# Kernel optimization log

Hardware: AMD Instinct MI355X
Metric: run time of the kernel (lower is better)

## Reference

```python
import jax, jax.numpy as jnp
import numpy as np

B, T, D, H, K = 8, 4096, 768, 12, 64
EPS_WKV = 1e-9
EPS_GN = 1e-5


def setup_inputs() -> dict:
    key = jax.random.key(0)
    ks = jax.random.split(key, 12)
    x = jax.random.normal(ks[0], (B, T, D), jnp.float32)
    # linear projection weights (torch nn.Linear stores [out, in]; y = x @ W.T)
    W_r = jax.random.normal(ks[1], (D, D), jnp.float32) * 0.02
    W_k = jax.random.normal(ks[2], (D, D), jnp.float32) * 0.02
    W_v = jax.random.normal(ks[3], (D, D), jnp.float32) * 0.02
    W_o = jax.random.normal(ks[4], (D, D), jnp.float32) * 0.02
    time_mix_r = jax.random.uniform(ks[5], (D,), jnp.float32)
    time_mix_k = jax.random.uniform(ks[6], (D,), jnp.float32)
    time_mix_v = jax.random.uniform(ks[7], (D,), jnp.float32)
    # around the module's init values (time_decay ~ -0.075, time_first ~ 0.15 at layer 6/12)
    time_decay = -0.075 + 0.1 * jax.random.normal(ks[8], (H, K), jnp.float32)
    time_first = 0.15 + 0.1 * jax.random.normal(ks[9], (H, K), jnp.float32)
    gn_weight = jnp.ones((D,), jnp.float32)
    gn_bias = jnp.zeros((D,), jnp.float32)
    return {
        "x": x,
        "time_mix_r": time_mix_r, "time_mix_k": time_mix_k, "time_mix_v": time_mix_v,
        "time_decay": time_decay, "time_first": time_first,
        "W_r": W_r, "W_k": W_k, "W_v": W_v, "W_o": W_o,
        "gn_weight": gn_weight, "gn_bias": gn_bias,
    }


def reference(x, time_mix_r, time_mix_k, time_mix_v, time_decay, time_first,
              W_r, W_k, W_v, W_o, gn_weight, gn_bias):
    Bx, Tx, Dx = x.shape
    Hx, Kx = time_decay.shape
    # token-shift: previous timestep (zero-initialized state)
    x_prev = jnp.concatenate([jnp.zeros_like(x[:, :1]), x[:, :-1]], axis=1)
    xr = x * time_mix_r + x_prev * (1.0 - time_mix_r)
    xk = x * time_mix_k + x_prev * (1.0 - time_mix_k)
    xv = x * time_mix_v + x_prev * (1.0 - time_mix_v)
    r = jax.nn.sigmoid(xr @ W_r.T).reshape(Bx, Tx, Hx, Kx)
    k = (xk @ W_k.T).reshape(Bx, Tx, Hx, Kx)
    v = (xv @ W_v.T).reshape(Bx, Tx, Hx, Kx)

    w = jnp.exp(-jnp.exp(time_decay))   # [H,K] decay per channel
    eu = jnp.exp(time_first)            # [H,K] bonus for current token

    def step(carry, kv_t):
        num, den = carry                # each [B,H,K]
        k_t, v_t = kv_t                 # each [B,H,K]
        ek = jnp.exp(k_t)
        wkv = (num + eu * ek * v_t) / (den + eu * ek + EPS_WKV)
        return (num * w + ek * v_t, den * w + ek), wkv

    k_tm = jnp.moveaxis(k, 1, 0)        # [T,B,H,K]
    v_tm = jnp.moveaxis(v, 1, 0)
    init = (jnp.zeros((Bx, Hx, Kx), x.dtype), jnp.zeros((Bx, Hx, Kx), x.dtype))
    _, wkv = jax.lax.scan(step, init, (k_tm, v_tm))
    out = jnp.moveaxis(wkv, 0, 1)       # [B,T,H,K]

    y = r * out                         # [B,T,H,K]
    # torch GroupNorm(H, D) on [B, D, T]: normalize each group over (K channels x T steps)
    mean = y.mean(axis=(1, 3), keepdims=True)
    var = y.var(axis=(1, 3), keepdims=True)
    y = (y - mean) * jax.lax.rsqrt(var + EPS_GN)
    y = y * gn_weight.reshape(1, 1, Hx, Kx) + gn_bias.reshape(1, 1, Hx, Kx)
    return y.reshape(Bx, Tx, Dx) @ W_o.T
```

## Files before the change

### kernel.cpp

```cpp
#include <hip/hip_runtime.h>
#include <hip/hip_bf16.h>
#include <cstdint>

#define B_ 8
#define T_ 4096
#define D_ 768
#define H_ 12
#define M_ (B_*T_)
#define CHUNKS 64
#define CLEN 64
#define WELEM (D_*D_)
#define NCH (B_*H_*64)

typedef __attribute__((ext_vector_type(8))) short bf16x8;
typedef __attribute__((ext_vector_type(4))) float f32x4;

static __device__ __forceinline__ unsigned short f2bf(float f) {
  __hip_bfloat16 h = __float2bfloat16(f);
  return __builtin_bit_cast(unsigned short, h);
}
static __device__ __forceinline__ float bf2f(unsigned short u) {
  unsigned v = ((unsigned)u) << 16;
  return __builtin_bit_cast(float, v);
}

static __device__ __forceinline__ void async16(const void* g, void* l) {
  __builtin_amdgcn_global_load_lds(
      (const __attribute__((address_space(1))) unsigned int*)g,
      (__attribute__((address_space(3))) unsigned int*)l, 16, 0, 0);
}

__global__ __launch_bounds__(256) void zero_out_kernel(float* __restrict__ out, size_t n4) {
  size_t gid = (size_t)blockIdx.x * 256 + threadIdx.x;
  if (gid < n4) *(float4*)(out + gid * 4) = make_float4(0.f, 0.f, 0.f, 0.f);
}

__global__ __launch_bounds__(256) void mix_kernel(
    const float* __restrict__ x, const float* __restrict__ tmr,
    const float* __restrict__ tmk, const float* __restrict__ tmv,
    unsigned short* __restrict__ xr, unsigned short* __restrict__ xk,
    unsigned short* __restrict__ xv) {
  size_t gid = (size_t)blockIdx.x * 256 + threadIdx.x;
  size_t idx4 = gid * 4;
  int d = (int)(idx4 % D_);
  size_t row = idx4 / D_;
  int t = (int)(row & (T_ - 1));
  float4 xc = *(const float4*)(x + idx4);
  float4 xp = make_float4(0.f, 0.f, 0.f, 0.f);
  if (t > 0) xp = *(const float4*)(x + idx4 - D_);
  float4 mr = *(const float4*)(tmr + d);
  float4 mk = *(const float4*)(tmk + d);
  float4 mv = *(const float4*)(tmv + d);
  ushort4 orr, okk, ovv;
  orr.x = f2bf(xc.x*mr.x + xp.x*(1.f-mr.x));
  orr.y = f2bf(xc.y*mr.y + xp.y*(1.f-mr.y));
  orr.z = f2bf(xc.z*mr.z + xp.z*(1.f-mr.z));
  orr.w = f2bf(xc.w*mr.w + xp.w*(1.f-mr.w));
  okk.x = f2bf(xc.x*mk.x + xp.x*(1.f-mk.x));
  okk.y = f2bf(xc.y*mk.y + xp.y*(1.f-mk.y));
  okk.z = f2bf(xc.z*mk.z + xp.z*(1.f-mk.z));
  okk.w = f2bf(xc.w*mk.w + xp.w*(1.f-mk.w));
  ovv.x = f2bf(xc.x*mv.x + xp.x*(1.f-mv.x));
  ovv.y = f2bf(xc.y*mv.y + xp.y*(1.f-mv.y));
  ovv.z = f2bf(xc.z*mv.z + xp.z*(1.f-mv.z));
  ovv.w = f2bf(xc.w*mv.w + xp.w*(1.f-mv.w));
  *(ushort4*)(xr + idx4) = orr;
  *(ushort4*)(xk + idx4) = okk;
  *(ushort4*)(xv + idx4) = ovv;
}

__global__ __launch_bounds__(256) void wconv_kernel(
    const float* __restrict__ a, const float* __restrict__ b,
    const float* __restrict__ c, const float* __restrict__ d,
    unsigned short* __restrict__ o) {
  size_t gid = (size_t)blockIdx.x * 256 + threadIdx.x;
  size_t idx4 = gid * 4;
  size_t mi = idx4 / WELEM;
  size_t off = idx4 % WELEM;
  const float* src = (mi == 0) ? a : (mi == 1) ? b : (mi == 2) ? c : d;
  float4 v = *(const float4*)(src + off);
  ushort4 u;
  u.x = f2bf(v.x); u.y = f2bf(v.y); u.z = f2bf(v.z); u.w = f2bf(v.w);
  *(ushort4*)(o + idx4) = u;
}

template<int ACT, int OBF>
__global__ __launch_bounds__(256) void gemm_nt(
    const unsigned short* __restrict__ A,
    const unsigned short* __restrict__ Bw,
    void* __restrict__ Cv, int M, int N, int Kd) {
  __shared__ __align__(16) unsigned short As[128 * 32];
  __shared__ __align__(16) unsigned short Bs[128 * 32];
  const int tid = threadIdx.x;
  const int wave = tid >> 6, lane = tid & 63;
  const int quad = lane >> 4, l16 = lane & 15;
  const int m0 = blockIdx.y * 128, n0 = blockIdx.x * 128;
  const int wm = (wave & 1) * 64, wn = (wave >> 1) * 64;

  f32x4 acc[4][4] = {};

  for (int kb = 0; kb < Kd; kb += 32) {
    __syncthreads();
#pragma unroll
    for (int j = 0; j < 2; ++j) {
      int chunk = wave * 128 + j * 64 + lane;
      int row = chunk >> 2, kc = chunk & 3;
      const unsigned short* ga = A  + ((size_t)(m0 + row) * Kd + kb + kc * 8);
      async16(ga, &As[chunk * 8]);
      const unsigned short* gb = Bw + ((size_t)(n0 + row) * Kd + kb + kc * 8);
      async16(gb, &Bs[chunk * 8]);
    }
    __syncthreads();

    bf16x8 a[4], b[4];
#pragma unroll
    for (int i = 0; i < 4; ++i)
      a[i] = *(const bf16x8*)&As[(wm + i * 16 + l16) * 32 + quad * 8];
#pragma unroll
    for (int i = 0; i < 4; ++i)
      b[i] = *(const bf16x8*)&Bs[(wn + i * 16 + l16) * 32 + quad * 8];
#pragma unroll
    for (int i = 0; i < 4; ++i)
#pragma unroll
      for (int j = 0; j < 4; ++j)
        acc[i][j] = __builtin_amdgcn_mfma_f32_16x16x32_bf16(a[i], b[j], acc[i][j], 0, 0, 0);
  }

#pragma unroll
  for (int i = 0; i < 4; ++i) {
    int rowb = m0 + wm + i * 16 + quad * 4;
#pragma unroll
    for (int j = 0; j < 4; ++j) {
      int col = n0 + wn + j * 16 + l16;
#pragma unroll
      for (int r = 0; r < 4; ++r) {
        float v = acc[i][j][r];
        if (ACT == 1) v = 1.f / (1.f + __expf(-v));
        size_t idx = (size_t)(rowb + r) * N + col;
        if (OBF) ((unsigned short*)Cv)[idx] = f2bf(v);
        else     ((float*)Cv)[idx] = v;
      }
    }
  }
}

__global__ __launch_bounds__(256) void wkv_pass1(
    const unsigned short* __restrict__ Kb, const unsigned short* __restrict__ Vb,
    const float* __restrict__ td,
    float* __restrict__ sumN, float* __restrict__ sumD) {
  int gid = blockIdx.x * 256 + threadIdx.x;
  int k = gid & 63;
  int h = (gid >> 6) % H_;
  int tmp = (gid >> 6) / H_;
  int b = tmp % B_;
  int c = tmp / B_;
  float w = __expf(-__expf(td[h * 64 + k]));
  size_t base = ((size_t)(b * T_ + c * CLEN)) * D_ + h * 64 + k;
  float num = 0.f, den = 0.f;
#pragma unroll 8
  for (int i = 0; i < CLEN; ++i) {
    float kk = bf2f(Kb[base + (size_t)i * D_]);
    float vv = bf2f(Vb[base + (size_t)i * D_]);
    float ek = __expf(kk);
    num = num * w + ek * vv;
    den = den * w + ek;
  }
  sumN[gid] = num;
  sumD[gid] = den;
}

__global__ __launch_bounds__(256) void wkv_pass2(
    const float* __restrict__ sumN, const float* __restrict__ sumD,
    const float* __restrict__ td,
    float* __restrict__ prefN, float* __restrict__ prefD,
    float* __restrict__ gstats) {
  int tid = blockIdx.x * 256 + threadIdx.x;
  if (blockIdx.x == 0 && threadIdx.x < 192) gstats[threadIdx.x] = 0.f;
  int k = tid & 63;
  int h = (tid >> 6) % H_;
  float w = __expf(-__expf(td[h * 64 + k]));
  float wL = w;
#pragma unroll
  for (int i = 0; i < 6; ++i) wL *= wL;
  float n = 0.f, d = 0.f;
  for (int c = 0; c < CHUNKS; ++c) {
    int j = c * NCH + tid;
    prefN[j] = n; prefD[j] = d;
    n = n * wL + sumN[j];
    d = d * wL + sumD[j];
  }
}

__global__ __launch_bounds__(256) void wkv_pass3(
    const unsigned short* __restrict__ Kb, const unsigned short* __restrict__ Vb,
    unsigned short* __restrict__ RY,
    const float* __restrict__ td, const float* __restrict__ tf,
    const float* __restrict__ prefN, const float* __restrict__ prefD,
    float* __restrict__ gsum, float* __restrict__ gsq) {
  int gid = blockIdx.x * 256 + threadIdx.x;
  int k = gid & 63;
  int h = (gid >> 6) % H_;
  int tmp = (gid >> 6) / H_;
  int b = tmp % B_;
  int c = tmp / B_;
  float w = __expf(-__expf(td[h * 64 + k]));
  float eu = __expf(tf[h * 64 + k]);
  float num = prefN[gid], den = prefD[gid];
  size_t base = ((size_t)(b * T_ + c * CLEN)) * D_ + h * 64 + k;
  float s1 = 0.f, s2 = 0.f;
#pragma unroll 4
  for (int i = 0; i < CLEN; ++i) {
    size_t idx = base + (size_t)i * D_;
    float kk = bf2f(Kb[idx]);
    float vv = bf2f(Vb[idx]);
    float rr = bf2f(RY[idx]);
    float ek = __expf(kk);
    float wkv = (num + eu * ek * vv) / (den + eu * ek + 1e-9f);
    unsigned short ybf = f2bf(rr * wkv);
    RY[idx] = ybf;
    float y = bf2f(ybf);
    s1 += y; s2 += y * y;
    num = num * w + ek * vv;
    den = den * w + ek;
  }
#pragma unroll
  for (int off = 32; off; off >>= 1) {
    s1 += __shfl_down(s1, off);
    s2 += __shfl_down(s2, off);
  }
  if (k == 0) {
    atomicAdd(&gsum[b * H_ + h], s1);
    atomicAdd(&gsq [b * H_ + h], s2);
  }
}

__global__ __launch_bounds__(256) void gn_kernel(
    const unsigned short* __restrict__ Y, const float* __restrict__ gsum,
    const float* __restrict__ gsq, const float* __restrict__ gw,
    const float* __restrict__ gb, unsigned short* __restrict__ Ybf) {
  size_t gid = (size_t)blockIdx.x * 256 + threadIdx.x;
  size_t idx4 = gid * 4;
  int d = (int)(idx4 % D_);
  size_t row = idx4 / D_;
  int b = (int)(row >> 12);
  int h = d >> 6;
  int g = b * H_ + h;
  const float inv = 1.f / (float)(T_ * 64);
  float mean = gsum[g] * inv;
  float var = gsq[g] * inv - mean * mean;
  float rstd = rsqrtf(var + 1e-5f);
  ushort4 yu = *(const ushort4*)(Y + idx4);
  float4 wv = *(const float4*)(gw + d);
  float4 bv = *(const float4*)(gb + d);
  ushort4 o;
  o.x = f2bf((bf2f(yu.x) - mean) * rstd * wv.x + bv.x);
  o.y = f2bf((bf2f(yu.y) - mean) * rstd * wv.y + bv.y);
  o.z = f2bf((bf2f(yu.z) - mean) * rstd * wv.z + bv.z);
  o.w = f2bf((bf2f(yu.w) - mean) * rstd * wv.w + bv.w);
  *(ushort4*)(Ybf + idx4) = o;
}

extern "C" void kernel_launch(void* const* d_in, const int* in_sizes, int n_in,
                              void* d_out, int out_size, void* d_ws, size_t ws_size,
                              hipStream_t stream) {
  (void)in_sizes; (void)n_in;
  const float* x   = (const float*)d_in[0];
  const float* tmr = (const float*)d_in[1];
  const float* tmk = (const float*)d_in[2];
  const float* tmv = (const float*)d_in[3];
  const float* td  = (const float*)d_in[4];
  const float* tf  = (const float*)d_in[5];
  const float* Wr  = (const float*)d_in[6];
  const float* Wk  = (const float*)d_in[7];
  const float* Wv  = (const float*)d_in[8];
  const float* Wo  = (const float*)d_in[9];
  const float* gw  = (const float*)d_in[10];
  const float* gb  = (const float*)d_in[11];
  float* out = (float*)d_out;

  constexpr size_t MD = (size_t)M_ * D_;
  constexpr size_t NEED = 4 * (MD * 2)
                        + (size_t)4 * WELEM * 2
                        + 4 * ((size_t)CHUNKS * NCH * 4)
                        + 1024;
  if (ws_size < NEED) {
    zero_out_kernel<<<(int)((MD / 4 + 255) / 256), 256, 0, stream>>>(out, MD / 4);
    return;
  }

  char* ws = (char*)d_ws;
  unsigned short* XR = (unsigned short*)ws; ws += MD * 2;
  unsigned short* XK = (unsigned short*)ws; ws += MD * 2;
  unsigned short* XV = (unsigned short*)ws; ws += MD * 2;
  unsigned short* Rb = (unsigned short*)ws; ws += MD * 2;
  unsigned short* Wb = (unsigned short*)ws; ws += (size_t)4 * WELEM * 2;
  float* sumN  = (float*)ws; ws += (size_t)CHUNKS * NCH * 4;
  float* sumD  = (float*)ws; ws += (size_t)CHUNKS * NCH * 4;
  float* prefN = (float*)ws; ws += (size_t)CHUNKS * NCH * 4;
  float* prefD = (float*)ws; ws += (size_t)CHUNKS * NCH * 4;
  float* gstats = (float*)ws; ws += 1024;
  unsigned short* Kb = XR;
  unsigned short* Vb = XK;
  unsigned short* Yb = XV;

  mix_kernel<<<(int)(MD / 1024), 256, 0, stream>>>(x, tmr, tmk, tmv, XR, XK, XV);
  wconv_kernel<<<(4 * WELEM / 4) / 256, 256, 0, stream>>>(Wr, Wk, Wv, Wo, Wb);

  dim3 ggrid(D_ / 128, M_ / 128);
  gemm_nt<1, 1><<<ggrid, 256, 0, stream>>>(XR, Wb,             Rb, M_, D_, D_);
  gemm_nt<0, 1><<<ggrid, 256, 0, stream>>>(XK, Wb + WELEM,     Kb, M_, D_, D_);
  gemm_nt<0, 1><<<ggrid, 256, 0, stream>>>(XV, Wb + 2 * WELEM, Vb, M_, D_, D_);

  wkv_pass1<<<(CHUNKS * NCH) / 256, 256, 0, stream>>>(Kb, Vb, td, sumN, sumD);
  wkv_pass2<<<NCH / 256, 256, 0, stream>>>(sumN, sumD, td, prefN, prefD, gstats);
  wkv_pass3<<<(CHUNKS * NCH) / 256, 256, 0, stream>>>(Kb, Vb, Rb, td, tf,
                                                      prefN, prefD, gstats, gstats + 96);
  gn_kernel<<<(int)(MD / 1024), 256, 0, stream>>>(Rb, gstats, gstats + 96, gw, gb, Yb);

  gemm_nt<0, 0><<<ggrid, 256, 0, stream>>>(Yb, Wb + 3 * WELEM, out, M_, D_, D_);
}
```

Measured before the change: 579.0 us.

## Fold token-shift mixing into concatenated weights and fuse R/K/V projections

After: 695.9 us. 20.2% more time.

```diff
diff --git a/kernel.cpp b/kernel.cpp
--- a/kernel.cpp
+++ b/kernel.cpp
@@ -9,8 +9,10 @@
 #define M_ (B_*T_)
 #define CHUNKS 64
 #define CLEN 64
-#define WELEM (D_*D_)
 #define NCH (B_*H_*64)
+#define KF 1536
+#define NF 2304
+#define TP1 (T_+1)
 
 typedef __attribute__((ext_vector_type(8))) short bf16x8;
 typedef __attribute__((ext_vector_type(4))) float f32x4;
@@ -35,118 +37,201 @@
   if (gid < n4) *(float4*)(out + gid * 4) = make_float4(0.f, 0.f, 0.f, 0.f);
 }
 
-__global__ __launch_bounds__(256) void mix_kernel(
-    const float* __restrict__ x, const float* __restrict__ tmr,
-    const float* __restrict__ tmk, const float* __restrict__ tmv,
-    unsigned short* __restrict__ xr, unsigned short* __restrict__ xk,
-    unsigned short* __restrict__ xv) {
+__global__ __launch_bounds__(256) void xpad_kernel(
+    const float* __restrict__ x, unsigned short* __restrict__ xp) {
   size_t gid = (size_t)blockIdx.x * 256 + threadIdx.x;
   size_t idx4 = gid * 4;
+  size_t row = idx4 / D_;
   int d = (int)(idx4 % D_);
-  size_t row = idx4 / D_;
-  int t = (int)(row & (T_ - 1));
-  float4 xc = *(const float4*)(x + idx4);
-  float4 xp = make_float4(0.f, 0.f, 0.f, 0.f);
-  if (t > 0) xp = *(const float4*)(x + idx4 - D_);
-  float4 mr = *(const float4*)(tmr + d);
-  float4 mk = *(const float4*)(tmk + d);
-  float4 mv = *(const float4*)(tmv + d);
-  ushort4 orr, okk, ovv;
-  orr.x = f2bf(xc.x*mr.x + xp.x*(1.f-mr.x));
-  orr.y = f2bf(xc.y*mr.y + xp.y*(1.f-mr.y));
-  orr.z = f2bf(xc.z*mr.z + xp.z*(1.f-mr.z));
-  orr.w = f2bf(xc.w*mr.w + xp.w*(1.f-mr.w));
-  okk.x = f2bf(xc.x*mk.x + xp.x*(1.f-mk.x));
-  okk.y = f2bf(xc.y*mk.y + xp.y*(1.f-mk.y));
-  okk.z = f2bf(xc.z*mk.z + xp.z*(1.f-mk.z));
-  okk.w = f2bf(xc.w*mk.w + xp.w*(1.f-mk.w));
-  ovv.x = f2bf(xc.x*mv.x + xp.x*(1.f-mv.x));
-  ovv.y = f2bf(xc.y*mv.y + xp.y*(1.f-mv.y));
-  ovv.z = f2bf(xc.z*mv.z + xp.z*(1.f-mv.z));
-  ovv.w = f2bf(xc.w*mv.w + xp.w*(1.f-mv.w));
-  *(ushort4*)(xr + idx4) = orr;
-  *(ushort4*)(xk + idx4) = okk;
-  *(ushort4*)(xv + idx4) = ovv;
-}
-
-__global__ __launch_bounds__(256) void wconv_kernel(
-    const float* __restrict__ a, const float* __restrict__ b,
-    const float* __restrict__ c, const float* __restrict__ d,
-    unsigned short* __restrict__ o) {
+  int b = (int)(row / TP1);
+  int tt = (int)(row % TP1);
+  ushort4 u = make_ushort4(0, 0, 0, 0);
+  if (tt > 0) {
+    float4 v = *(const float4*)(x + ((size_t)(b * T_ + tt - 1)) * D_ + d);
+    u.x = f2bf(v.x); u.y = f2bf(v.y); u.z = f2bf(v.z); u.w = f2bf(v.w);
+  }
+  *(ushort4*)(xp + idx4) = u;
+}
+
+__global__ __launch_bounds__(256) void wfold_kernel(
+    const float* __restrict__ Wr, const float* __restrict__ Wk,
+    const float* __restrict__ Wv,
+    const float* __restrict__ tmr, const float* __restrict__ tmk,
+    const float* __restrict__ tmv, unsigned short* __restrict__ Wcat) {
   size_t gid = (size_t)blockIdx.x * 256 + threadIdx.x;
   size_t idx4 = gid * 4;
-  size_t mi = idx4 / WELEM;
-  size_t off = idx4 % WELEM;
-  const float* src = (mi == 0) ? a : (mi == 1) ? b : (mi == 2) ? c : d;
-  float4 v = *(const float4*)(src + off);
+  int j = (int)(idx4 % KF);
+  int n = (int)(idx4 / KF);
+  int which = n / D_;
+  int nn = n % D_;
+  const float* W = (which == 0) ? Wr : (which == 1) ? Wk : Wv;
+  const float* mx = (which == 0) ? tmr : (which == 1) ? tmk : tmv;
+  int cur = (j < D_);
+  int jj = cur ? j : j - D_;
+  float4 wv = *(const float4*)(W + (size_t)nn * D_ + jj);
+  float4 mv = *(const float4*)(mx + jj);
+  float4 f;
+  f.x = cur ? mv.x : (1.f - mv.x);
+  f.y = cur ? mv.y : (1.f - mv.y);
+  f.z = cur ? mv.z : (1.f - mv.z);
+  f.w = cur ? mv.w : (1.f - mv.w);
+  ushort4 u;
+  u.x = f2bf(wv.x * f.x); u.y = f2bf(wv.y * f.y);
+  u.z = f2bf(wv.z * f.z); u.w = f2bf(wv.w * f.w);
+  *(ushort4*)(Wcat + idx4) = u;
+}
+
+__global__ __launch_bounds__(256) void woconv_kernel(
+    const float* __restrict__ w, unsigned short* __restrict__ o) {
+  size_t gid = (size_t)blockIdx.x * 256 + threadIdx.x;
+  size_t idx4 = gid * 4;
+  float4 v = *(const float4*)(w + idx4);
   ushort4 u;
   u.x = f2bf(v.x); u.y = f2bf(v.y); u.z = f2bf(v.z); u.w = f2bf(v.w);
   *(ushort4*)(o + idx4) = u;
 }
 
-template<int ACT, int OBF>
-__global__ __launch_bounds__(256) void gemm_nt(
-    const unsigned short* __restrict__ A,
-    const unsigned short* __restrict__ Bw,
-    void* __restrict__ Cv, int M, int N, int Kd) {
-  __shared__ __align__(16) unsigned short As[128 * 32];
-  __shared__ __align__(16) unsigned short Bs[128 * 32];
+__global__ __launch_bounds__(256) void gemm_fused(
+    const unsigned short* __restrict__ xpad,
+    const unsigned short* __restrict__ Wcat,
+    unsigned short* __restrict__ RKV) {
+  __shared__ __align__(16) unsigned short smem[128 * 128];
+  unsigned short* As = smem;
+  unsigned short* Bs = smem + 128 * 32;
+
+  const int flat = blockIdx.x;
+  const int xcd = flat & 7;
+  const int j8 = flat >> 3;
+  const int strip = xcd * 32 + j8 / 18;
+  const int ntile = j8 % 18;
+  const int m0 = strip * 128, n0 = ntile * 128;
+  const int b = strip >> 5;
+  const int tbase = (strip & 31) * 128;
+
   const int tid = threadIdx.x;
   const int wave = tid >> 6, lane = tid & 63;
   const int quad = lane >> 4, l16 = lane & 15;
-  const int m0 = blockIdx.y * 128, n0 = blockIdx.x * 128;
   const int wm = (wave & 1) * 64, wn = (wave >> 1) * 64;
 
+  const size_t bbase = (size_t)b * TP1 * D_;
+
   f32x4 acc[4][4] = {};
 
-  for (int kb = 0; kb < Kd; kb += 32) {
+  for (int kb = 0; kb < KF; kb += 32) {
     __syncthreads();
 #pragma unroll
-    for (int j = 0; j < 2; ++j) {
-      int chunk = wave * 128 + j * 64 + lane;
+    for (int jj = 0; jj < 2; ++jj) {
+      int chunk = wave * 128 + jj * 64 + lane;
       int row = chunk >> 2, kc = chunk & 3;
-      const unsigned short* ga = A  + ((size_t)(m0 + row) * Kd + kb + kc * 8);
+      int kg = kb + kc * 8;
+      int cur = (kg < D_);
+      int kk = cur ? kg : kg - D_;
+      const unsigned short* ga =
+          xpad + bbase + ((size_t)(tbase + row + cur)) * D_ + kk;
       async16(ga, &As[chunk * 8]);
-      const unsigned short* gb = Bw + ((size_t)(n0 + row) * Kd + kb + kc * 8);
+      const unsigned short* gb = Wcat + ((size_t)(n0 + row)) * KF + kg;
       async16(gb, &Bs[chunk * 8]);
     }
     __syncthreads();
 
-    bf16x8 a[4], b[4];
+    bf16x8 a[4], bfr[4];
 #pragma unroll
     for (int i = 0; i < 4; ++i)
       a[i] = *(const bf16x8*)&As[(wm + i * 16 + l16) * 32 + quad * 8];
 #pragma unroll
     for (int i = 0; i < 4; ++i)
-      b[i] = *(const bf16x8*)&Bs[(wn + i * 16 + l16) * 32 + quad * 8];
-#pragma unroll
-    for (int i = 0; i < 4; ++i)
-#pragma unroll
-      for (int j = 0; j < 4; ++j)
-        acc[i][j] = __builtin_amdgcn_mfma_f32_16x16x32_bf16(a[i], b[j], acc[i][j], 0, 0, 0);
+      bfr[i] = *(const bf16x8*)&Bs[(wn + i * 16 + l16) * 32 + quad * 8];
+#pragma unroll
+    for (int i = 0; i < 4; ++i)
+#pragma unroll
+      for (int jj = 0; jj < 4; ++jj)
+        acc[i][jj] = __builtin_amdgcn_mfma_f32_16x16x32_bf16(a[i], bfr[jj], acc[i][jj], 0, 0, 0);
+  }
+
+  const int do_sig = (ntile < 6);
+  __syncthreads();
+#pragma unroll
+  for (int i = 0; i < 4; ++i)
+#pragma unroll
+    for (int jj = 0; jj < 4; ++jj)
+#pragma unroll
+      for (int r = 0; r < 4; ++r) {
+        float v = acc[i][jj][r];
+        if (do_sig) v = 1.f / (1.f + __expf(-v));
+        smem[(wm + i * 16 + quad * 4 + r) * 128 + wn + jj * 16 + l16] = f2bf(v);
+      }
+  __syncthreads();
+#pragma unroll
+  for (int s = 0; s < 8; ++s) {
+    int cid = s * 256 + tid;
+    int row = cid >> 4, c8 = cid & 15;
+    bf16x8 val = *(const bf16x8*)&smem[row * 128 + c8 * 8];
+    *(bf16x8*)(RKV + (size_t)(m0 + row) * NF + n0 + c8 * 8) = val;
+  }
+}
+
+__global__ __launch_bounds__(256) void gemm_wo(
+    const unsigned short* __restrict__ A,
+    const unsigned short* __restrict__ Bw,
+    float* __restrict__ C) {
+  __shared__ __align__(16) unsigned short As[128 * 32];
+  __shared__ __align__(16) unsigned short Bs[128 * 32];
+  const int flat = blockIdx.x;
+  const int xcd = flat & 7;
+  const int j8 = flat >> 3;
+  const int strip = xcd * 32 + j8 / 6;
+  const int ntile = j8 % 6;
+  const int m0 = strip * 128, n0 = ntile * 128;
+
+  const int tid = threadIdx.x;
+  const int wave = tid >> 6, lane = tid & 63;
+  const int quad = lane >> 4, l16 = lane & 15;
+  const int wm = (wave & 1) * 64, wn = (wave >> 1) * 64;
+
+  f32x4 acc[4][4] = {};
+
+  for (int kb = 0; kb < D_; kb += 32) {
+    __syncthreads();
+#pragma unroll
+    for (int jj = 0; jj < 2; ++jj) {
+      int chunk = wave * 128 + jj * 64 + lane;
+      int row = chunk >> 2, kc = chunk & 3;
+      const unsigned short* ga = A + ((size_t)(m0 + row)) * D_ + kb + kc * 8;
+      async16(ga, &As[chunk * 8]);
+      const unsigned short* gb = Bw + ((size_t)(n0 + row)) * D_ + kb + kc * 8;
+      async16(gb, &Bs[chunk * 8]);
+    }
+    __syncthreads();
+
+    bf16x8 a[4], bfr[4];
+#pragma unroll
+    for (int i = 0; i < 4; ++i)
+      a[i] = *(const bf16x8*)&As[(wm + i * 16 + l16) * 32 + quad * 8];
+#pragma unroll
+    for (int i = 0; i < 4; ++i)
+      bfr[i] = *(const bf16x8*)&Bs[(wn + i * 16 + l16) * 32 + quad * 8];
+#pragma unroll
+    for (int i = 0; i < 4; ++i)
+#pragma unroll
+      for (int jj = 0; jj < 4; ++jj)
+        acc[i][jj] = __builtin_amdgcn_mfma_f32_16x16x32_bf16(a[i], bfr[jj], acc[i][jj], 0, 0, 0);
   }
 
 #pragma unroll
   for (int i = 0; i < 4; ++i) {
     int rowb = m0 + wm + i * 16 + quad * 4;
 #pragma unroll
-    for (int j = 0; j < 4; ++j) {
-      int col = n0 + wn + j * 16 + l16;
-#pragma unroll
-      for (int r = 0; r < 4; ++r) {
-        float v = acc[i][j][r];
-        if (ACT == 1) v = 1.f / (1.f + __expf(-v));
-        size_t idx = (size_t)(rowb + r) * N + col;
-        if (OBF) ((unsigned short*)Cv)[idx] = f2bf(v);
-        else     ((float*)Cv)[idx] = v;
-      }
+    for (int jj = 0; jj < 4; ++jj) {
+      int col = n0 + wn + jj * 16 + l16;
+#pragma unroll
+      for (int r = 0; r < 4; ++r)
+        C[(size_t)(rowb + r) * D_ + col] = acc[i][jj][r];
     }
   }
 }
 
 __global__ __launch_bounds__(256) void wkv_pass1(
-    const unsigned short* __restrict__ Kb, const unsigned short* __restrict__ Vb,
-    const float* __restrict__ td,
+    const unsigned short* __restrict__ RKV, const float* __restrict__ td,
     float* __restrict__ sumN, float* __restrict__ sumD) {
   int gid = blockIdx.x * 256 + threadIdx.x;
   int k = gid & 63;
@@ -155,12 +240,13 @@
   int b = tmp % B_;
   int c = tmp / B_;
   float w = __expf(-__expf(td[h * 64 + k]));
-  size_t base = ((size_t)(b * T_ + c * CLEN)) * D_ + h * 64 + k;
+  const unsigned short* Kp =
+      RKV + ((size_t)(b * T_ + c * CLEN)) * NF + D_ + h * 64 + k;
   float num = 0.f, den = 0.f;
 #pragma unroll 8
   for (int i = 0; i < CLEN; ++i) {
-    float kk = bf2f(Kb[base + (size_t)i * D_]);
-    float vv = bf2f(Vb[base + (size_t)i * D_]);
+    float kk = bf2f(Kp[(size_t)i * NF]);
+    float vv = bf2f(Kp[(size_t)i * NF + D_]);
     float ek = __expf(kk);
     num = num * w + ek * vv;
     den = den * w + ek;
@@ -170,10 +256,8 @@
 }
 
 __global__ __launch_bounds__(256) void wkv_pass2(
-    const float* __restrict__ sumN, const float* __restrict__ sumD,
-    const float* __restrict__ td,
-    float* __restrict__ prefN, float* __restrict__ prefD,
-    float* __restrict__ gstats) {
+    float* __restrict__ sumN, float* __restrict__ sumD,
+    const float* __restrict__ td, float* __restrict__ gstats) {
   int tid = blockIdx.x * 256 + threadIdx.x;
   if (blockIdx.x == 0 && threadIdx.x < 192) gstats[threadIdx.x] = 0.f;
   int k = tid & 63;
@@ -185,15 +269,15 @@
   float n = 0.f, d = 0.f;
   for (int c = 0; c < CHUNKS; ++c) {
     int j = c * NCH + tid;
-    prefN[j] = n; prefD[j] = d;
-    n = n * wL + sumN[j];
-    d = d * wL + sumD[j];
+    float sn = sumN[j], sd = sumD[j];
+    sumN[j] = n; sumD[j] = d;
+    n = n * wL + sn;
+    d = d * wL + sd;
   }
 }
 
 __global__ __launch_bounds__(256) void wkv_pass3(
-    const unsigned short* __restrict__ Kb, const unsigned short* __restrict__ Vb,
-    unsigned short* __restrict__ RY,
+    unsigned short* __restrict__ RKV,
     const float* __restrict__ td, const float* __restrict__ tf,
     const float* __restrict__ prefN, const float* __restrict__ prefD,
     float* __restrict__ gsum, float* __restrict__ gsq) {
@@ -206,18 +290,18 @@
   float w = __expf(-__expf(td[h * 64 + k]));
   float eu = __expf(tf[h * 64 + k]);
   float num = prefN[gid], den = prefD[gid];
-  size_t base = ((size_t)(b * T_ + c * CLEN)) * D_ + h * 64 + k;
+  unsigned short* Rp = RKV + ((size_t)(b * T_ + c * CLEN)) * NF + h * 64 + k;
   float s1 = 0.f, s2 = 0.f;
 #pragma unroll 4
   for (int i = 0; i < CLEN; ++i) {
-    size_t idx = base + (size_t)i * D_;
-    float kk = bf2f(Kb[idx]);
-    float vv = bf2f(Vb[idx]);
-    float rr = bf2f(RY[idx]);
+    size_t off = (size_t)i * NF;
+    float rr = bf2f(Rp[off]);
+    float kk = bf2f(Rp[off + D_]);
+    float vv = bf2f(Rp[off + 2 * D_]);
     float ek = __expf(kk);
     float wkv = (num + eu * ek * vv) / (den + eu * ek + 1e-9f);
     unsigned short ybf = f2bf(rr * wkv);
-    RY[idx] = ybf;
+    Rp[off] = ybf;
     float y = bf2f(ybf);
     s1 += y; s2 += y * y;
     num = num * w + ek * vv;
@@ -235,9 +319,9 @@
 }
 
 __global__ __launch_bounds__(256) void gn_kernel(
-    const unsigned short* __restrict__ Y, const float* __restrict__ gsum,
+    const unsigned short* __restrict__ RKV, const float* __restrict__ gsum,
     const float* __restrict__ gsq, const float* __restrict__ gw,
-    const float* __restrict__ gb, unsigned short* __restrict__ Ybf) {
+    const float* __restrict__ gb, unsigned short* __restrict__ Yb) {
   size_t gid = (size_t)blockIdx.x * 256 + threadIdx.x;
   size_t idx4 = gid * 4;
   int d = (int)(idx4 % D_);
@@ -249,7 +333,7 @@
   float mean = gsum[g] * inv;
   float var = gsq[g] * inv - mean * mean;
   float rstd = rsqrtf(var + 1e-5f);
-  ushort4 yu = *(const ushort4*)(Y + idx4);
+  ushort4 yu = *(const ushort4*)(RKV + row * NF + d);
   float4 wv = *(const float4*)(gw + d);
   float4 bv = *(const float4*)(gb + d);
   ushort4 o;
@@ -257,13 +341,13 @@
   o.y = f2bf((bf2f(yu.y) - mean) * rstd * wv.y + bv.y);
   o.z = f2bf((bf2f(yu.z) - mean) * rstd * wv.z + bv.z);
   o.w = f2bf((bf2f(yu.w) - mean) * rstd * wv.w + bv.w);
-  *(ushort4*)(Ybf + idx4) = o;
+  *(ushort4*)(Yb + idx4) = o;
 }
 
 extern "C" void kernel_launch(void* const* d_in, const int* in_sizes, int n_in,
                               void* d_out, int out_size, void* d_ws, size_t ws_size,
                               hipStream_t stream) {
-  (void)in_sizes; (void)n_in;
+  (void)in_sizes; (void)n_in; (void)out_size;
   const float* x   = (const float*)d_in[0];
   const float* tmr = (const float*)d_in[1];
   const float* tmk = (const float*)d_in[2];
@@ -278,44 +362,38 @@
   const float* gb  = (const float*)d_in[11];
   float* out = (float*)d_out;
 
-  constexpr size_t MD = (size_t)M_ * D_;
-  constexpr size_t NEED = 4 * (MD * 2)
-                        + (size_t)4 * WELEM * 2
-                        + 4 * ((size_t)CHUNKS * NCH * 4)
-                        + 1024;
+  constexpr size_t XPAD_E = (size_t)B_ * TP1 * D_;
+  constexpr size_t RKV_E  = (size_t)M_ * NF;
+  constexpr size_t WCAT_E = (size_t)NF * KF;
+  constexpr size_t WO_E   = (size_t)D_ * D_;
+  constexpr size_t MD     = (size_t)M_ * D_;
+  constexpr size_t NEED   = 2 * (XPAD_E + RKV_E + WCAT_E + WO_E);
   if (ws_size < NEED) {
     zero_out_kernel<<<(int)((MD / 4 + 255) / 256), 256, 0, stream>>>(out, MD / 4);
     return;
   }
 
   char* ws = (char*)d_ws;
-  unsigned short* XR = (unsigned short*)ws; ws += MD * 2;
-  unsigned short* XK = (unsigned short*)ws; ws += MD * 2;
-  unsigned short* XV = (unsigned short*)ws; ws += MD * 2;
-  unsigned short* Rb = (unsigned short*)ws; ws += MD * 2;
-  unsigned short* Wb = (unsigned short*)ws; ws += (size_t)4 * WELEM * 2;
-  float* sumN  = (float*)ws; ws += (size_t)CHUNKS * NCH * 4;
-  float* sumD  = (float*)ws; ws += (size_t)CHUNKS * NCH * 4;
-  float* prefN = (float*)ws; ws += (size_t)CHUNKS * NCH * 4;
-  float* prefD = (float*)ws; ws += (size_t)CHUNKS * NCH * 4;
-  float* gstats = (float*)ws; ws += 1024;
-  unsigned short* Kb = XR;
-  unsigned short* Vb = XK;
-  unsigned short* Yb = XV;
-
-  mix_kernel<<<(int)(MD / 1024), 256, 0, stream>>>(x, tmr, tmk, tmv, XR, XK, XV);
-  wconv_kernel<<<(4 * WELEM / 4) / 256, 256, 0, stream>>>(Wr, Wk, Wv, Wo, Wb);
-
-  dim3 ggrid(D_ / 128, M_ / 128);
-  gemm_nt<1, 1><<<ggrid, 256, 0, stream>>>(XR, Wb,             Rb, M_, D_, D_);
-  gemm_nt<0, 1><<<ggrid, 256, 0, stream>>>(XK, Wb + WELEM,     Kb, M_, D_, D_);
-  gemm_nt<0, 1><<<ggrid, 256, 0, stream>>>(XV, Wb + 2 * WELEM, Vb, M_, D_, D_);
-
-  wkv_pass1<<<(CHUNKS * NCH) / 256, 256, 0, stream>>>(Kb, Vb, td, sumN, sumD);
-  wkv_pass2<<<NCH / 256, 256, 0, stream>>>(sumN, sumD, td, prefN, prefD, gstats);
-  wkv_pass3<<<(CHUNKS * NCH) / 256, 256, 0, stream>>>(Kb, Vb, Rb, td, tf,
-                                                      prefN, prefD, gstats, gstats + 96);
-  gn_kernel<<<(int)(MD / 1024), 256, 0, stream>>>(Rb, gstats, gstats + 96, gw, gb, Yb);
-
-  gemm_nt<0, 0><<<ggrid, 256, 0, stream>>>(Yb, Wb + 3 * WELEM, out, M_, D_, D_);
-}
+  unsigned short* Xp   = (unsigned short*)ws; ws += XPAD_E * 2;
+  unsigned short* RKV  = (unsigned short*)ws; ws += RKV_E * 2;
+  unsigned short* Wcat = (unsigned short*)ws; ws += WCAT_E * 2;
+  unsigned short* Wob  = (unsigned short*)ws; ws += WO_E * 2;
+  unsigned short* Yb = Xp;
+  float* sumN   = (float*)Wcat;
+  float* sumD   = sumN + (size_t)CHUNKS * NCH;
+  float* gstats = sumD + (size_t)CHUNKS * NCH;
+
+  xpad_kernel <<<(int)(XPAD_E / 1024), 256, 0, stream>>>(x, Xp);
+  wfold_kernel<<<(int)(WCAT_E / 1024), 256, 0, stream>>>(Wr, Wk, Wv, tmr, tmk, tmv, Wcat);
+  woconv_kernel<<<(int)(WO_E / 1024), 256, 0, stream>>>(Wo, Wob);
+
+  gemm_fused<<<8 * 32 * 18, 256, 0, stream>>>(Xp, Wcat, RKV);
+
+  wkv_pass1<<<(CHUNKS * NCH) / 256, 256, 0, stream>>>(RKV, td, sumN, sumD);
+  wkv_pass2<<<NCH / 256, 256, 0, stream>>>(sumN, sumD, td, gstats);
+  wkv_pass3<<<(CHUNKS * NCH) / 256, 256, 0, stream>>>(RKV, td, tf, sumN, sumD,
+                                                      gstats, gstats + 96);
+  gn_kernel<<<(int)(MD / 1024), 256, 0, stream>>>(RKV, gstats, gstats + 96, gw, gb, Yb);
+
+  gemm_wo<<<8 * 32 * 6, 256, 0, stream>>>(Yb, Wob, out);
+}
```
